# Performance work log

Measured on AMD Instinct MI355X. Metric: run time of the kernel, lower is better.

The kernel has to match this reference:

```python
import jax, jax.numpy as jnp
import numpy as np

B, S, IN, H, NC, WSEG = 2, 256, 80, 128, 40, 64
F2 = 2 * H  # bidirectional LSTM output dim


def setup_inputs() -> dict:
    key = jax.random.key(0)
    it = iter(jax.random.split(key, 48))
    def nrm(shape, scale):
        return jax.random.normal(next(it), shape, jnp.float32) * scale
    d = {}
    d["x"] = jax.random.normal(next(it), (B, S, IN), jnp.float32)
    d["lengths"] = jnp.full((B,), S, dtype=jnp.int32)
    ins = [IN, F2]
    for l in range(2):
        for dr in ("f", "b"):
            sc = 1.0 / np.sqrt(H)
            d[f"w_ih_l{l}{dr}"] = nrm((4 * H, ins[l]), sc)
            d[f"w_hh_l{l}{dr}"] = nrm((4 * H, H), sc)
            d[f"b_l{l}{dr}"] = nrm((4 * H,), sc)
    PD = 3 * F2  # pairwise phi feature dim
    d["a_s0"] = jnp.float32(0.25); d["w_s1"] = nrm((100, PD), 1.0 / np.sqrt(PD)); d["b_s1"] = jnp.zeros((100,), jnp.float32)
    d["a_s1"] = jnp.float32(0.25); d["w_s2"] = nrm((1, 100), 0.1); d["b_s2"] = jnp.zeros((1,), jnp.float32)
    d["a_c0"] = jnp.float32(0.25); d["w_c1"] = nrm((2 * NC, F2), 1.0 / np.sqrt(F2)); d["b_c1"] = jnp.zeros((2 * NC,), jnp.float32)
    d["a_c1"] = jnp.float32(0.25); d["w_c2"] = nrm((NC, 2 * NC), 0.1); d["b_c2"] = jnp.zeros((NC,), jnp.float32)
    d["a_b0"] = jnp.float32(0.25); d["w_b1"] = nrm((2 * NC, F2), 1.0 / np.sqrt(F2)); d["b_b1"] = jnp.zeros((2 * NC,), jnp.float32)
    d["a_b1"] = jnp.float32(0.25); d["w_b2"] = nrm((2, 2 * NC), 0.1); d["b_b2"] = jnp.zeros((2,), jnp.float32)
    return d


def prelu(x, a):
    return jnp.where(x >= 0, x, a * x)


def mlp(x, a0, W1, b1, a1, W2, b2):
    h = prelu(x, a0) @ W1.T + b1
    return prelu(h, a1) @ W2.T + b2


def lstm_dir(x, Wih, Whh, b, reverse):
    # PyTorch gate order: i, f, g, o
    pre = jnp.einsum("bsi,gi->sbg", x, Wih) + b  # [S,B,4H]
    if reverse:
        pre = pre[::-1]
    h0 = jnp.zeros((x.shape[0], Whh.shape[1]), x.dtype)
    def step(carry, xt):
        h, c = carry
        g = xt + h @ Whh.T
        i, f, gg, o = jnp.split(g, 4, axis=-1)
        c = jax.nn.sigmoid(f) * c + jax.nn.sigmoid(i) * jnp.tanh(gg)
        h = jax.nn.sigmoid(o) * jnp.tanh(c)
        return (h, c), h
    _, hs = jax.lax.scan(step, (h0, h0), pre)
    if reverse:
        hs = hs[::-1]
    return jnp.swapaxes(hs, 0, 1)  # [B,S,H]


def encode(x, layers):
    out = x
    for (wif, whf, bf, wib, whb, bb) in layers:
        out = jnp.concatenate([
            lstm_dir(out, wif, whf, bf, False),
            lstm_dir(out, wib, whb, bb, True),
        ], axis=-1)
    return out


def compute_scores(rnn_out, a_s0, w_s1, b_s1, a_s1, w_s2, b_s2):
    cum = jnp.cumsum(rnn_out, axis=1)
    # phi[b,i,j] = [cum[j]-cum[i], out[i], out[j]]  (faithful to calc_phi)
    c = cum[:, None, :, :] - cum[:, :, None, :]
    sh = c.shape
    dmat = jnp.broadcast_to(rnn_out[:, :, None, :], sh)
    emat = jnp.broadcast_to(rnn_out[:, None, :, :], sh)
    phi = jnp.concatenate([c, dmat, emat], axis=-1)  # [B,S,S,3*F2]
    return mlp(phi, a_s0, w_s1, b_s1, a_s1, w_s2, b_s2)[..., 0]  # [B,S,S]


def dp_backptr(scores):
    # Viterbi-style DP: best[i] = max_{j in [i-WSEG, i)} best[j] + scores[:, j, i]
    Bn, Sn = scores.shape[:2]
    def step(best, i):
        start = jnp.maximum(0, i - WSEG)
        jidx = start + jnp.arange(WSEG)
        bwin = jax.lax.dynamic_slice(best, (0, start), (Bn, WSEG))
        swin = jax.lax.dynamic_slice(scores, (0, start, i), (Bn, WSEG, 1))[..., 0]
        cand = jnp.where(jidx[None, :] < i, bwin + swin, -1e9)
        k = (start + jnp.argmax(cand, axis=1)).astype(jnp.int32)
        best = jax.lax.dynamic_update_slice(best, jnp.max(cand, axis=1, keepdims=True), (0, i))
        return best, k
    _, ks = jax.lax.scan(step, jnp.zeros((Bn, Sn), scores.dtype), jnp.arange(1, Sn))
    backptr = jnp.concatenate([jnp.zeros((1, Bn), jnp.int32), ks], axis=0).T  # [B,S]
    return backptr


def backtrack(scores, backptr, lengths):
    Bn, Sn = scores.shape[:2]
    bar = jnp.arange(Bn)
    def step(carry, _):
        cur, acc, bm = carry
        bm = bm.at[bar, cur].set(True)
        prev = backptr[bar, cur]
        active = cur > 0
        acc = acc + jnp.where(active, scores[bar, prev, cur], 0.0)
        cur = jnp.where(active, prev, 0)
        return (cur, acc, bm), None
    init = ((lengths - 1).astype(jnp.int32), jnp.zeros((Bn,), scores.dtype), jnp.zeros((Bn, Sn), bool))
    (_, acc, bm), _ = jax.lax.scan(step, init, None, length=Sn)
    return bm, acc


def reference(x, lengths,
              w_ih_l0f, w_hh_l0f, b_l0f, w_ih_l0b, w_hh_l0b, b_l0b,
              w_ih_l1f, w_hh_l1f, b_l1f, w_ih_l1b, w_hh_l1b, b_l1b,
              a_s0, w_s1, b_s1, a_s1, w_s2, b_s2,
              a_c0, w_c1, b_c1, a_c1, w_c2, b_c2,
              a_b0, w_b1, b_b1, a_b1, w_b2, b_b2):
    layers = [
        (w_ih_l0f, w_hh_l0f, b_l0f, w_ih_l0b, w_hh_l0b, b_l0b),
        (w_ih_l1f, w_hh_l1f, b_l1f, w_ih_l1b, w_hh_l1b, b_l1b),
    ]
    rnn_out = encode(x, layers)  # [B,S,2H]
    cls_out = mlp(rnn_out, a_c0, w_c1, b_c1, a_c1, w_c2, b_c2)
    bin_out = mlp(rnn_out, a_b0, w_b1, b_b1, a_b1, w_b2, b_b2)
    scores = compute_scores(rnn_out, a_s0, w_s1, b_s1, a_s1, w_s2, b_s2)
    backptr = dp_backptr(scores)
    bmask, pred_scores = backtrack(scores, backptr, lengths)
    # bmask[b,i]==1 iff i is a predicted segment boundary (padded-dense encoding of pred lists)
    return cls_out, bin_out, bmask.astype(jnp.int32), pred_scores
```

## Files before the change

### kernel.cpp

```cpp
#include <hip/hip_runtime.h>
#include <math.h>


#define OFF_BIN 20480
#define OFF_BM  21504
#define OFF_PRED 22016

__device__ __forceinline__ float preluf(float x, float a) { return x >= 0.f ? x : a * x; }
__device__ __forceinline__ float sigf(float x) { return 1.f / (1.f + __expf(-x)); }
__device__ __forceinline__ float tanh_fast(float x) { return 1.f - 2.f / (__expf(2.f * x) + 1.f); }

__global__ __launch_bounds__(256) void k_gemm(const float* __restrict__ A,
                                              const float* __restrict__ B,
                                              int Adim, int K,
                                              const float* __restrict__ wf,
                                              const float* __restrict__ bf,
                                              const float* __restrict__ wb,
                                              const float* __restrict__ bbv,
                                              float* __restrict__ outF,
                                              float* __restrict__ outB) {
    int mtile = blockIdx.y;
    int dir = mtile >> 3;
    const float* W = dir ? wb : wf;
    const float* bias = dir ? bbv : bf;
    float* out = dir ? outB : outF;
    int g0 = (mtile & 7) << 6;
    int tb0 = blockIdx.x << 6;
    int tid = threadIdx.x;
    int Bdim = K - Adim;

    __shared__ float Ws[16][68];
    __shared__ float Xs[16][68];

    int r = tid >> 2, c4 = tid & 3;
    int tbr = tb0 + r;
    int hr = ((tbr & 1) << 8) | (tbr >> 1);
    int ty = tid >> 4;
    int tx = tid & 15;
    float acc[4][4] = {};

    for (int k0 = 0; k0 < K; k0 += 16) {
        float4 wv = *(const float4*)(W + (size_t)(g0 + r) * K + k0 + (c4 << 2));
        const float* src = (k0 < Adim) ? (A + (size_t)hr * Adim + k0)
                                       : (B + (size_t)hr * Bdim + (k0 - Adim));
        float4 xv = *(const float4*)(src + (c4 << 2));
        __syncthreads();
        int kc = c4 << 2;
        Ws[kc + 0][r] = wv.x; Ws[kc + 1][r] = wv.y; Ws[kc + 2][r] = wv.z; Ws[kc + 3][r] = wv.w;
        Xs[kc + 0][r] = xv.x; Xs[kc + 1][r] = xv.y; Xs[kc + 2][r] = xv.z; Xs[kc + 3][r] = xv.w;
        __syncthreads();
#pragma unroll
        for (int kk = 0; kk < 16; ++kk) {
            float4 wq = *(const float4*)&Ws[kk][ty << 2];
            float4 xq = *(const float4*)&Xs[kk][tx << 2];
            acc[0][0] += wq.x * xq.x; acc[0][1] += wq.x * xq.y; acc[0][2] += wq.x * xq.z; acc[0][3] += wq.x * xq.w;
            acc[1][0] += wq.y * xq.x; acc[1][1] += wq.y * xq.y; acc[1][2] += wq.y * xq.z; acc[1][3] += wq.y * xq.w;
            acc[2][0] += wq.z * xq.x; acc[2][1] += wq.z * xq.y; acc[2][2] += wq.z * xq.z; acc[2][3] += wq.z * xq.w;
            acc[3][0] += wq.w * xq.x; acc[3][1] += wq.w * xq.y; acc[3][2] += wq.w * xq.z; acc[3][3] += wq.w * xq.w;
        }
    }
    int gq = g0 + (ty << 2);
    float b0 = bias[gq], b1 = bias[gq + 1], b2 = bias[gq + 2], b3 = bias[gq + 3];
#pragma unroll
    for (int j = 0; j < 4; ++j) {
        int tb = tb0 + (tx << 2) + j;
        float4 v = make_float4(acc[0][j] + b0, acc[1][j] + b1, acc[2][j] + b2, acc[3][j] + b3);
        *(float4*)(out + (size_t)tb * 512 + gq) = v;
    }
}

__global__ __launch_bounds__(512, 2) void k_lstm(const float* __restrict__ pre_f,
                                                 const float* __restrict__ pre_b,
                                                 const float* __restrict__ whh_f,
                                                 const float* __restrict__ whh_b,
                                                 float* __restrict__ hout_f,
                                                 float* __restrict__ hout_b) {
    const int dir = blockIdx.x >> 1;
    const int b = blockIdx.x & 1;
    const float* pre = dir ? pre_b : pre_f;
    const float* whh = dir ? whh_b : whh_f;
    float* hout = dir ? hout_b : hout_f;
    const int tid = threadIdx.x;
    const int c = tid >> 7;
    const int gg = tid & 127;
    const int k0 = c << 5;

    float w[4][32];
#pragma unroll
    for (int j = 0; j < 4; ++j) {
#pragma unroll
        for (int k = 0; k < 32; k += 4) {
            float4 v = *(const float4*)(whh + (size_t)((j << 7) + gg) * 128 + k0 + k);
            w[j][k] = v.x; w[j][k + 1] = v.y; w[j][k + 2] = v.z; w[j][k + 3] = v.w;
        }
    }

    __shared__ __align__(16) float hl[128];
    __shared__ float4 part[4][128];
    if (tid < 128) hl[tid] = 0.f;
    float cst = 0.f;
    __syncthreads();

    int t0 = dir ? 255 : 0;
    const float* pp0 = pre + ((size_t)t0 * 2 + b) * 512;
    float p0 = pp0[gg], p1 = pp0[128 + gg], p2 = pp0[256 + gg], p3 = pp0[384 + gg];

    for (int step = 0; step < 256; ++step) {
        int t = dir ? (255 - step) : step;
        float n0 = 0.f, n1 = 0.f, n2 = 0.f, n3 = 0.f;
        if (step < 255) {
            int tn = dir ? (254 - step) : (step + 1);
            const float* pp = pre + ((size_t)tn * 2 + b) * 512;
            n0 = pp[gg]; n1 = pp[128 + gg]; n2 = pp[256 + gg]; n3 = pp[384 + gg];
        }
        float a0 = 0.f, a1 = 0.f, a2 = 0.f, a3 = 0.f;
#pragma unroll
        for (int k = 0; k < 32; k += 4) {
            float4 h4 = *(const float4*)(hl + k0 + k);
            a0 += w[0][k] * h4.x + w[0][k + 1] * h4.y + w[0][k + 2] * h4.z + w[0][k + 3] * h4.w;
            a1 += w[1][k] * h4.x + w[1][k + 1] * h4.y + w[1][k + 2] * h4.z + w[1][k + 3] * h4.w;
            a2 += w[2][k] * h4.x + w[2][k + 1] * h4.y + w[2][k + 2] * h4.z + w[2][k + 3] * h4.w;
            a3 += w[3][k] * h4.x + w[3][k + 1] * h4.y + w[3][k + 2] * h4.z + w[3][k + 3] * h4.w;
        }
        part[c][gg] = make_float4(a0, a1, a2, a3);
        __syncthreads();
        float4 q0 = part[0][gg], q1 = part[1][gg], q2 = part[2][gg], q3 = part[3][gg];
        float gi = p0 + ((q0.x + q1.x) + (q2.x + q3.x));
        float gf = p1 + ((q0.y + q1.y) + (q2.y + q3.y));
        float gG = p2 + ((q0.z + q1.z) + (q2.z + q3.z));
        float go = p3 + ((q0.w + q1.w) + (q2.w + q3.w));
        cst = sigf(gf) * cst + sigf(gi) * tanh_fast(gG);
        float h = sigf(go) * tanh_fast(cst);
        hl[gg] = h;
        if (tid < 128) hout[(size_t)(((b << 8) + t) << 7) + gg] = h;
        p0 = n0; p1 = n1; p2 = n2; p3 = n3;
        __syncthreads();
    }
}

__global__ __launch_bounds__(256) void k_feats(const float* __restrict__ h1f,
                                               const float* __restrict__ h1b,
                                               const float* __restrict__ ws1,
                                               const float* __restrict__ bs1,
                                               const float* a_s0,
                                               float* __restrict__ Pd,
                                               float* __restrict__ Pe,
                                               const float* ac0p, const float* __restrict__ wc1,
                                               const float* __restrict__ bc1, const float* ac1p,
                                               const float* __restrict__ wc2, const float* __restrict__ bc2,
                                               const float* ab0p, const float* __restrict__ wb1,
                                               const float* __restrict__ bb1, const float* ab1p,
                                               const float* __restrict__ wb2, const float* __restrict__ bb2,
                                               float* __restrict__ out,
                                               float* __restrict__ cum) {
    __shared__ __align__(16) float xa[256];
    __shared__ __align__(16) float xb2[256];
    __shared__ __align__(16) float hc[80];
    __shared__ __align__(16) float hb[80];
    int bid = blockIdx.x;
    int tid = threadIdx.x;
    int kk = tid & 127;
    if (bid < 512) {
        int row = bid;
        float a0 = a_s0[0];
        float v = ((tid < 128) ? h1f : h1b)[(size_t)row * 128 + kk];
        xa[tid] = preluf(v, a0);
        __syncthreads();
        const float4* p4 = (const float4*)xa;
        if (tid < 100) {
            const float4* wr = (const float4*)(ws1 + (size_t)tid * 768 + 256);
            float acc = bs1[tid];
#pragma unroll 8
            for (int q = 0; q < 64; ++q) {
                float4 w4 = wr[q], x4 = p4[q];
                acc += w4.x * x4.x + w4.y * x4.y + w4.z * x4.z + w4.w * x4.w;
            }
            Pd[(size_t)row * 100 + tid] = acc;
        } else if (tid >= 128 && tid < 228) {
            int u = tid - 128;
            const float4* wr = (const float4*)(ws1 + (size_t)u * 768 + 512);
            float acc = 0.f;
#pragma unroll 8
            for (int q = 0; q < 64; ++q) {
                float4 w4 = wr[q], x4 = p4[q];
                acc += w4.x * x4.x + w4.y * x4.y + w4.z * x4.z + w4.w * x4.w;
            }
            Pe[(size_t)row * 100 + u] = acc;
        }
    } else if (bid < 1024) {
        int row = bid - 512;
        float ac0 = ac0p[0], ac1 = ac1p[0], ab0 = ab0p[0], ab1 = ab1p[0];
        float v = ((tid < 128) ? h1f : h1b)[(size_t)row * 128 + kk];
        xa[tid] = preluf(v, ac0);
        xb2[tid] = preluf(v, ab0);
        __syncthreads();
        if (tid < 80) {
            const float4* wr = (const float4*)(wc1 + (size_t)tid * 256);
            const float4* x4 = (const float4*)xa;
            float acc = bc1[tid];
#pragma unroll 8
            for (int q = 0; q < 64; ++q) {
                float4 w4 = wr[q], p = x4[q];
                acc += w4.x * p.x + w4.y * p.y + w4.z * p.z + w4.w * p.w;
            }
            hc[tid] = preluf(acc, ac1);
        } else if (tid >= 128 && tid < 208) {
            int u = tid - 128;
            const float4* wr = (const float4*)(wb1 + (size_t)u * 256);
            const float4* x4 = (const float4*)xb2;
            float acc = bb1[u];
#pragma unroll 8
            for (int q = 0; q < 64; ++q) {
                float4 w4 = wr[q], p = x4[q];
                acc += w4.x * p.x + w4.y * p.y + w4.z * p.z + w4.w * p.w;
            }
            hb[u] = preluf(acc, ab1);
        }
        __syncthreads();
        if (tid < 40) {
            const float4* wr = (const float4*)(wc2 + (size_t)tid * 80);
            const float4* h4 = (const float4*)hc;
            float acc = bc2[tid];
#pragma unroll
            for (int q = 0; q < 20; ++q) {
                float4 w4 = wr[q], p = h4[q];
                acc += w4.x * p.x + w4.y * p.y + w4.z * p.z + w4.w * p.w;
            }
            out[(size_t)row * 40 + tid] = acc;
        } else if (tid >= 64 && tid < 66) {
            int j = tid - 64;
            const float4* wr = (const float4*)(wb2 + (size_t)j * 80);
            const float4* h4 = (const float4*)hb;
            float acc = bb2[j];
#pragma unroll
            for (int q = 0; q < 20; ++q) {
                float4 w4 = wr[q], p = h4[q];
                acc += w4.x * p.x + w4.y * p.y + w4.z * p.z + w4.w * p.w;
            }
            out[OFF_BIN + (size_t)row * 2 + j] = acc;
        }
    } else {
        int b = bid - 1024;
        const float* src = (tid < 128) ? h1f : h1b;
        float run = 0.f;
#pragma unroll 8
        for (int t = 0; t < 256; ++t) {
            float v = src[(size_t)(((b << 8) + t) << 7) + kk];
            cum[(size_t)(((b << 8) + t) << 8) + tid] = run + v;
            run += v;
        }
    }
}

__global__ __launch_bounds__(256) void k_scores(const float* __restrict__ cum,
                                                const float* __restrict__ ws1,
                                                const float* __restrict__ ws2,
                                                const float* __restrict__ bs2,
                                                const float* __restrict__ Pd,
                                                const float* __restrict__ Pe,
                                                const float* a_s0p, const float* a_s1p,
                                                float* __restrict__ scT) {
    int bid = blockIdx.x;
    int dt = bid & 3, e = (bid >> 2) & 255, b = bid >> 10;
    int d0 = dt << 6;
    int tid = threadIdx.x;
    __shared__ float cume[256];
    __shared__ float Y[64 * 257];
    __shared__ float red[4][64];
    float a0 = a_s0p[0], a1 = a_s1p[0];
    cume[tid] = cum[(size_t)(((b << 8) + e) << 8) + tid];
    __syncthreads();
#pragma unroll 4
    for (int dj = 0; dj < 64; ++dj) {
        float cd = cum[(size_t)(((b << 8) + (d0 + dj)) << 8) + tid];
        Y[dj * 257 + tid] = preluf(cume[tid] - cd, a0);
    }
    __syncthreads();
    int ug = __builtin_amdgcn_readfirstlane(tid >> 6);
    int ld = tid & 63;
    int d = d0 + ld;
    float acc[25];
#pragma unroll
    for (int t = 0; t < 25; ++t) acc[t] = 0.f;
    const float* wc = ws1 + (size_t)(ug * 25) * 768;
    const float* yrow = Y + ld * 257;
    for (int k = 0; k < 256; k += 4) {
        float y0 = yrow[k], y1 = yrow[k + 1], y2 = yrow[k + 2], y3 = yrow[k + 3];
#pragma unroll
        for (int t = 0; t < 25; ++t) {
            float4 wq = *(const float4*)(wc + (size_t)t * 768 + k);
            acc[t] += y0 * wq.x + y1 * wq.y + y2 * wq.z + y3 * wq.w;
        }
    }
    const float* pdrow = Pd + (size_t)((b << 8) + d) * 100;
    const float* perow = Pe + (size_t)((b << 8) + e) * 100;
    float part = 0.f;
#pragma unroll
    for (int t = 0; t < 25; ++t) {
        int u = ug * 25 + t;
        float h = acc[t] + pdrow[u] + perow[u];
        part += preluf(h, a1) * ws2[u];
    }
    red[ug][ld] = part;
    __syncthreads();
    if (tid < 64) {
        float s = red[0][tid] + red[1][tid] + red[2][tid] + red[3][tid] + bs2[0];
        scT[(size_t)(((b << 8) + e) << 8) + d0 + tid] = s;
    }
}

__global__ __launch_bounds__(128) void k_dp(const float* __restrict__ scT,
                                            const int* __restrict__ lengths,
                                            float* __restrict__ out) {
    __shared__ float best[2][256];
    __shared__ int bp[2][256];
    __shared__ float bm[2][256];
    int tid = threadIdx.x;
    for (int i = tid; i < 512; i += 128) {
        ((float*)best)[i] = 0.f;
        ((int*)bp)[i] = 0;
        ((float*)bm)[i] = 0.f;
    }
    __syncthreads();
    int b = tid >> 6, ln = tid & 63;
    const float* sb = scT + ((size_t)b << 16);
    float sc_next = sb[(1 << 8) + ln];
    for (int i = 1; i < 256; ++i) {
        float sc = sc_next;
        if (i < 255) {
            int i2 = i + 1;
            int st2 = (i2 > 64) ? (i2 - 64) : 0;
            sc_next = sb[(i2 << 8) + st2 + ln];
        }
        int start = (i > 64) ? (i - 64) : 0;
        int j = start + ln;
        float v = -1000000000.0f;
        int ki = j;
        if (j < i) v = best[b][j] + sc;
#pragma unroll
        for (int off = 32; off > 0; off >>= 1) {
            float ov = __shfl_down(v, off);
            int ok = __shfl_down(ki, off);
            if (ov > v || (ov == v && ok < ki)) { v = ov; ki = ok; }
        }
        if (ln == 0) { best[b][i] = v; bp[b][i] = ki; }
    }
    __syncthreads();
    if (tid < 2) {
        int bb = tid;
        int cur = lengths[bb] - 1;
        out[OFF_PRED + bb] = best[bb][cur];
        for (int it = 0; it < 256; ++it) {
            bm[bb][cur] = 1.f;
            int prev = bp[bb][cur];
            cur = (cur > 0) ? prev : 0;
        }
    }
    __syncthreads();
    for (int i = tid; i < 512; i += 128) out[OFF_BM + i] = ((float*)bm)[i];
}

extern "C" void kernel_launch(void* const* d_in, const int* in_sizes, int n_in,
                              void* d_out, int out_size, void* d_ws, size_t ws_size,
                              hipStream_t stream) {
    const float* x     = (const float*)d_in[0];
    const int* lengths = (const int*)d_in[1];
    const float* wih0f = (const float*)d_in[2];
    const float* whh0f = (const float*)d_in[3];
    const float* b0f   = (const float*)d_in[4];
    const float* wih0b = (const float*)d_in[5];
    const float* whh0b = (const float*)d_in[6];
    const float* b0b   = (const float*)d_in[7];
    const float* wih1f = (const float*)d_in[8];
    const float* whh1f = (const float*)d_in[9];
    const float* b1f   = (const float*)d_in[10];
    const float* wih1b = (const float*)d_in[11];
    const float* whh1b = (const float*)d_in[12];
    const float* b1b   = (const float*)d_in[13];
    const float* a_s0  = (const float*)d_in[14];
    const float* w_s1  = (const float*)d_in[15];
    const float* b_s1  = (const float*)d_in[16];
    const float* a_s1  = (const float*)d_in[17];
    const float* w_s2  = (const float*)d_in[18];
    const float* b_s2  = (const float*)d_in[19];
    const float* a_c0  = (const float*)d_in[20];
    const float* w_c1  = (const float*)d_in[21];
    const float* b_c1  = (const float*)d_in[22];
    const float* a_c1  = (const float*)d_in[23];
    const float* w_c2  = (const float*)d_in[24];
    const float* b_c2  = (const float*)d_in[25];
    const float* a_b0  = (const float*)d_in[26];
    const float* w_b1  = (const float*)d_in[27];
    const float* b_b1  = (const float*)d_in[28];
    const float* a_b1  = (const float*)d_in[29];
    const float* w_b2  = (const float*)d_in[30];
    const float* b_b2  = (const float*)d_in[31];

    float* wsf = (float*)d_ws;
    float* preF = wsf;
    float* preB = wsf + 262144;
    float* h0f  = wsf + 524288;
    float* h0b  = wsf + 589824;
    float* h1f  = wsf + 655360;
    float* h1b  = wsf + 720896;
    float* cum  = wsf + 786432;
    float* Pd   = wsf + 917504;
    float* Pe   = wsf + 968704;
    float* scT  = wsf + 1019904;
    float* out  = (float*)d_out;

    k_gemm<<<dim3(8, 16), 256, 0, stream>>>(x, x, 80, 80, wih0f, b0f, wih0b, b0b, preF, preB);
    k_lstm<<<4, 512, 0, stream>>>(preF, preB, whh0f, whh0b, h0f, h0b);
    k_gemm<<<dim3(8, 16), 256, 0, stream>>>(h0f, h0b, 128, 256, wih1f, b1f, wih1b, b1b, preF, preB);
    k_lstm<<<4, 512, 0, stream>>>(preF, preB, whh1f, whh1b, h1f, h1b);
    k_feats<<<1026, 256, 0, stream>>>(h1f, h1b, w_s1, b_s1, a_s0, Pd, Pe,
                                      a_c0, w_c1, b_c1, a_c1, w_c2, b_c2,
                                      a_b0, w_b1, b_b1, a_b1, w_b2, b_b2, out, cum);
    k_scores<<<2048, 256, 0, stream>>>(cum, w_s1, w_s2, b_s2, Pd, Pe, a_s0, a_s1, scT);
    k_dp<<<1, 128, 0, stream>>>(scT, lengths, out);
}
```

Before: 1.025 ms.

## Restructure LSTM recurrence to one gate row per thread with shuffle-based gate combine

Each thread now holds a full 128-wide row of the recurrent weight matrix in registers and computes one gate pre-activation for one hidden unit. The four gates of a unit are combined with cross-lane shuffles, which removes the shared-memory partial-sum reduction. The hidden state is double-buffered in shared memory, so each time step needs one barrier instead of two. This is meant to shorten the latency of the serial 256-step critical path, at the cost of 128 weight registers per thread under a 512-thread, 2-block launch bound, which risks register spills.

```diff
diff --git a/kernel.cpp b/kernel.cpp
--- a/kernel.cpp
+++ b/kernel.cpp
@@ -81,60 +81,59 @@
     const float* whh = dir ? whh_b : whh_f;
     float* hout = dir ? hout_b : hout_f;
     const int tid = threadIdx.x;
-    const int c = tid >> 7;
-    const int gg = tid & 127;
-    const int k0 = c << 5;
-
-    float w[4][32];
-#pragma unroll
-    for (int j = 0; j < 4; ++j) {
-#pragma unroll
-        for (int k = 0; k < 32; k += 4) {
-            float4 v = *(const float4*)(whh + (size_t)((j << 7) + gg) * 128 + k0 + k);
-            w[j][k] = v.x; w[j][k + 1] = v.y; w[j][k + 2] = v.z; w[j][k + 3] = v.w;
-        }
-    }
-
-    __shared__ __align__(16) float hl[128];
-    __shared__ float4 part[4][128];
-    if (tid < 128) hl[tid] = 0.f;
+    const int wv = tid >> 6;
+    const int lane = tid & 63;
+    const int j = lane >> 4;
+    const int uu = (wv << 4) | (lane & 15);
+    const int row = (j << 7) | uu;
+
+    float w[128];
+#pragma unroll
+    for (int k = 0; k < 128; k += 4) {
+        float4 v = *(const float4*)(whh + (size_t)row * 128 + k);
+        w[k] = v.x; w[k + 1] = v.y; w[k + 2] = v.z; w[k + 3] = v.w;
+    }
+
+    __shared__ __align__(16) float hl[2][128];
+    if (tid < 128) hl[0][tid] = 0.f;
     float cst = 0.f;
     __syncthreads();
 
     int t0 = dir ? 255 : 0;
-    const float* pp0 = pre + ((size_t)t0 * 2 + b) * 512;
-    float p0 = pp0[gg], p1 = pp0[128 + gg], p2 = pp0[256 + gg], p3 = pp0[384 + gg];
-
+    float p = pre[((size_t)t0 * 2 + b) * 512 + row];
+
+    int buf = 0;
     for (int step = 0; step < 256; ++step) {
         int t = dir ? (255 - step) : step;
-        float n0 = 0.f, n1 = 0.f, n2 = 0.f, n3 = 0.f;
+        float n = 0.f;
         if (step < 255) {
             int tn = dir ? (254 - step) : (step + 1);
-            const float* pp = pre + ((size_t)tn * 2 + b) * 512;
-            n0 = pp[gg]; n1 = pp[128 + gg]; n2 = pp[256 + gg]; n3 = pp[384 + gg];
-        }
-        float a0 = 0.f, a1 = 0.f, a2 = 0.f, a3 = 0.f;
-#pragma unroll
-        for (int k = 0; k < 32; k += 4) {
-            float4 h4 = *(const float4*)(hl + k0 + k);
-            a0 += w[0][k] * h4.x + w[0][k + 1] * h4.y + w[0][k + 2] * h4.z + w[0][k + 3] * h4.w;
-            a1 += w[1][k] * h4.x + w[1][k + 1] * h4.y + w[1][k + 2] * h4.z + w[1][k + 3] * h4.w;
-            a2 += w[2][k] * h4.x + w[2][k + 1] * h4.y + w[2][k + 2] * h4.z + w[2][k + 3] * h4.w;
-            a3 += w[3][k] * h4.x + w[3][k + 1] * h4.y + w[3][k + 2] * h4.z + w[3][k + 3] * h4.w;
-        }
-        part[c][gg] = make_float4(a0, a1, a2, a3);
-        __syncthreads();
-        float4 q0 = part[0][gg], q1 = part[1][gg], q2 = part[2][gg], q3 = part[3][gg];
-        float gi = p0 + ((q0.x + q1.x) + (q2.x + q3.x));
-        float gf = p1 + ((q0.y + q1.y) + (q2.y + q3.y));
-        float gG = p2 + ((q0.z + q1.z) + (q2.z + q3.z));
-        float go = p3 + ((q0.w + q1.w) + (q2.w + q3.w));
-        cst = sigf(gf) * cst + sigf(gi) * tanh_fast(gG);
-        float h = sigf(go) * tanh_fast(cst);
-        hl[gg] = h;
-        if (tid < 128) hout[(size_t)(((b << 8) + t) << 7) + gg] = h;
-        p0 = n0; p1 = n1; p2 = n2; p3 = n3;
-        __syncthreads();
+            n = pre[((size_t)tn * 2 + b) * 512 + row];
+        }
+        float acc = p;
+#pragma unroll
+        for (int k = 0; k < 128; k += 4) {
+            float4 h4 = *(const float4*)(hl[buf] + k);
+            acc += w[k] * h4.x + w[k + 1] * h4.y + w[k + 2] * h4.z + w[k + 3] * h4.w;
+        }
+        float v = (j == 2) ? tanh_fast(acc) : sigf(acc);
+        float pv = __shfl_xor(v, 32);
+        float a = v * pv;
+        float sf = (j == 1) ? v : pv;
+        float so = (j == 1) ? pv : v;
+        float x1 = __shfl_xor((j & 1) ? sf : a, 16);
+        float x2 = __shfl_xor((j & 1) ? so : a, 16);
+        cst = x1 * cst + a;
+        float h = x2 * tanh_fast(cst);
+        if (j == 0) {
+            hl[buf ^ 1][uu] = h;
+            hout[(size_t)(((b << 8) + t) << 7) + uu] = h;
+        } else if (j == 2) {
+            hl[buf ^ 1][uu] = h;
+        }
+        p = n;
+        __syncthreads();
+        buf ^= 1;
     }
 }
 
```

Result: slower. 1.089 ms (+6.3%).

## Process two end positions per block in scores and use DPP argmax in DP

Applied to the files above, without the earlier changes.

The scores kernel now handles two e rows per block and computes the PReLU pairwise features on the fly from cached cum rows, so each w_s1 float4 load feeds two accumulators and the grid is halved. The DP kernel keeps the sliding window of best values in registers, replaces shuffle-based argmax with DPP row and broadcast ops plus readlane, and drops the shared best array. This trades extra register pressure (50 accumulators) for fewer global weight loads and shorter serial DP steps, and the DPP reduction must keep the same lowest-index tie-break.

```diff
diff --git a/kernel.cpp b/kernel.cpp
--- a/kernel.cpp
+++ b/kernel.cpp
@@ -261,95 +261,141 @@
                                                 const float* a_s0p, const float* a_s1p,
                                                 float* __restrict__ scT) {
     int bid = blockIdx.x;
-    int dt = bid & 3, e = (bid >> 2) & 255, b = bid >> 10;
-    int d0 = dt << 6;
+    int dt = bid & 3, et = (bid >> 2) & 127, b = bid >> 9;
+    int d0 = dt << 6, e0 = et << 1;
     int tid = threadIdx.x;
-    __shared__ float cume[256];
-    __shared__ float Y[64 * 257];
-    __shared__ float red[4][64];
+    __shared__ float cumd[64][260];
+    __shared__ __align__(16) float cume[2][260];
+    __shared__ float red[4][2][64];
     float a0 = a_s0p[0], a1 = a_s1p[0];
-    cume[tid] = cum[(size_t)(((b << 8) + e) << 8) + tid];
-    __syncthreads();
-#pragma unroll 4
-    for (int dj = 0; dj < 64; ++dj) {
-        float cd = cum[(size_t)(((b << 8) + (d0 + dj)) << 8) + tid];
-        Y[dj * 257 + tid] = preluf(cume[tid] - cd, a0);
-    }
-    __syncthreads();
+    {
+        int r = tid >> 2, q = tid & 3;
+        const float4* src = (const float4*)(cum + (size_t)(((b << 8) + (d0 + r)) << 8) + (q << 6));
+        float4* dst = (float4*)&cumd[r][q << 6];
+#pragma unroll
+        for (int x = 0; x < 16; ++x) dst[x] = src[x];
+    }
+    if (tid < 128) {
+        int er = tid >> 6, kq = tid & 63;
+        float4 v = *((const float4*)(cum + (size_t)(((b << 8) + (e0 + er)) << 8)) + kq);
+        *((float4*)&cume[er][0] + kq) = v;
+    }
+    __syncthreads();
+
     int ug = __builtin_amdgcn_readfirstlane(tid >> 6);
     int ld = tid & 63;
-    int d = d0 + ld;
-    float acc[25];
-#pragma unroll
-    for (int t = 0; t < 25; ++t) acc[t] = 0.f;
+    float acc0[25], acc1[25];
+#pragma unroll
+    for (int t = 0; t < 25; ++t) { acc0[t] = 0.f; acc1[t] = 0.f; }
     const float* wc = ws1 + (size_t)(ug * 25) * 768;
-    const float* yrow = Y + ld * 257;
     for (int k = 0; k < 256; k += 4) {
-        float y0 = yrow[k], y1 = yrow[k + 1], y2 = yrow[k + 2], y3 = yrow[k + 3];
+        float4 cd = *(const float4*)&cumd[ld][k];
+        float4 c0 = *(const float4*)&cume[0][k];
+        float4 c1 = *(const float4*)&cume[1][k];
+        float4 y0, y1;
+        y0.x = preluf(c0.x - cd.x, a0); y0.y = preluf(c0.y - cd.y, a0);
+        y0.z = preluf(c0.z - cd.z, a0); y0.w = preluf(c0.w - cd.w, a0);
+        y1.x = preluf(c1.x - cd.x, a0); y1.y = preluf(c1.y - cd.y, a0);
+        y1.z = preluf(c1.z - cd.z, a0); y1.w = preluf(c1.w - cd.w, a0);
 #pragma unroll
         for (int t = 0; t < 25; ++t) {
             float4 wq = *(const float4*)(wc + (size_t)t * 768 + k);
-            acc[t] += y0 * wq.x + y1 * wq.y + y2 * wq.z + y3 * wq.w;
-        }
-    }
-    const float* pdrow = Pd + (size_t)((b << 8) + d) * 100;
-    const float* perow = Pe + (size_t)((b << 8) + e) * 100;
-    float part = 0.f;
-#pragma unroll
-    for (int t = 0; t < 25; ++t) {
-        int u = ug * 25 + t;
-        float h = acc[t] + pdrow[u] + perow[u];
-        part += preluf(h, a1) * ws2[u];
-    }
-    red[ug][ld] = part;
-    __syncthreads();
-    if (tid < 64) {
-        float s = red[0][tid] + red[1][tid] + red[2][tid] + red[3][tid] + bs2[0];
-        scT[(size_t)(((b << 8) + e) << 8) + d0 + tid] = s;
-    }
+            acc0[t] += y0.x * wq.x + y0.y * wq.y + y0.z * wq.z + y0.w * wq.w;
+            acc1[t] += y1.x * wq.x + y1.y * wq.y + y1.z * wq.z + y1.w * wq.w;
+        }
+    }
+    const float* pdrow = Pd + (size_t)((b << 8) + d0 + ld) * 100;
+    {
+        const float* perow = Pe + (size_t)((b << 8) + e0) * 100;
+        float part = 0.f;
+#pragma unroll
+        for (int t = 0; t < 25; ++t) {
+            int u = ug * 25 + t;
+            float h = acc0[t] + pdrow[u] + perow[u];
+            part += preluf(h, a1) * ws2[u];
+        }
+        red[ug][0][ld] = part;
+    }
+    {
+        const float* perow = Pe + (size_t)((b << 8) + e0 + 1) * 100;
+        float part = 0.f;
+#pragma unroll
+        for (int t = 0; t < 25; ++t) {
+            int u = ug * 25 + t;
+            float h = acc1[t] + pdrow[u] + perow[u];
+            part += preluf(h, a1) * ws2[u];
+        }
+        red[ug][1][ld] = part;
+    }
+    __syncthreads();
+    if (tid < 128) {
+        int e = tid >> 6, l2 = tid & 63;
+        float s = red[0][e][l2] + red[1][e][l2] + red[2][e][l2] + red[3][e][l2] + bs2[0];
+        scT[(size_t)(((b << 8) + (e0 + e)) << 8) + d0 + l2] = s;
+    }
+}
+
+__device__ __forceinline__ void argmax_dpp(float& v, int& ki) {
+#define AD_STEP(CTRL, RMASK)                                                                    \
+    {                                                                                           \
+        int mv = __builtin_amdgcn_update_dpp(__float_as_int(v), __float_as_int(v), CTRL, RMASK, 0xf, false); \
+        int mk = __builtin_amdgcn_update_dpp(ki, ki, CTRL, RMASK, 0xf, false);                  \
+        float fv = __int_as_float(mv);                                                          \
+        bool take = (fv > v) || (fv == v && mk < ki);                                           \
+        v = take ? fv : v;                                                                      \
+        ki = take ? mk : ki;                                                                    \
+    }
+    AD_STEP(0x111, 0xf)
+    AD_STEP(0x112, 0xf)
+    AD_STEP(0x114, 0xf)
+    AD_STEP(0x118, 0xf)
+    AD_STEP(0x142, 0xa)
+    AD_STEP(0x143, 0xc)
+#undef AD_STEP
 }
 
 __global__ __launch_bounds__(128) void k_dp(const float* __restrict__ scT,
                                             const int* __restrict__ lengths,
                                             float* __restrict__ out) {
-    __shared__ float best[2][256];
     __shared__ int bp[2][256];
     __shared__ float bm[2][256];
     int tid = threadIdx.x;
     for (int i = tid; i < 512; i += 128) {
-        ((float*)best)[i] = 0.f;
         ((int*)bp)[i] = 0;
         ((float*)bm)[i] = 0.f;
     }
     __syncthreads();
     int b = tid >> 6, ln = tid & 63;
     const float* sb = scT + ((size_t)b << 16);
-    float sc_next = sb[(1 << 8) + ln];
+    int lenm1 = lengths[b] - 1;
+    float wreg = 0.f;
+    float bestFinal = 0.f;
+    int jcur = (ln < 1) ? ln : ln - 64;
+    float sc_next = sb[(1 << 8) + ((jcur < 0) ? 0 : jcur)];
     for (int i = 1; i < 256; ++i) {
         float sc = sc_next;
+        int j = jcur;
         if (i < 255) {
-            int i2 = i + 1;
-            int st2 = (i2 > 64) ? (i2 - 64) : 0;
-            sc_next = sb[(i2 << 8) + st2 + ln];
-        }
-        int start = (i > 64) ? (i - 64) : 0;
-        int j = start + ln;
-        float v = -1000000000.0f;
+            int m2 = (i + 1) & 63;
+            int base2 = (i + 1) - m2;
+            int j2 = (ln < m2) ? (base2 + ln) : (base2 + ln - 64);
+            jcur = j2;
+            sc_next = sb[((i + 1) << 8) + ((j2 < 0) ? 0 : j2)];
+        }
+        float v = (j >= 0) ? (wreg + sc) : -1000000000.0f;
         int ki = j;
-        if (j < i) v = best[b][j] + sc;
-#pragma unroll
-        for (int off = 32; off > 0; off >>= 1) {
-            float ov = __shfl_down(v, off);
-            int ok = __shfl_down(ki, off);
-            if (ov > v || (ov == v && ok < ki)) { v = ov; ki = ok; }
-        }
-        if (ln == 0) { best[b][i] = v; bp[b][i] = ki; }
-    }
+        argmax_dpp(v, ki);
+        float bv = __uint_as_float(__builtin_amdgcn_readlane(__float_as_uint(v), 63));
+        int bk = __builtin_amdgcn_readlane(ki, 63);
+        if (ln == (i & 63)) wreg = bv;
+        if (ln == 0) bp[b][i] = bk;
+        if (i == lenm1) bestFinal = bv;
+    }
+    if (ln == 0) out[OFF_PRED + b] = bestFinal;
     __syncthreads();
     if (tid < 2) {
         int bb = tid;
         int cur = lengths[bb] - 1;
-        out[OFF_PRED + bb] = best[bb][cur];
         for (int it = 0; it < 256; ++it) {
             bm[bb][cur] = 1.f;
             int prev = bp[bb][cur];
@@ -416,6 +462,6 @@
     k_feats<<<1026, 256, 0, stream>>>(h1f, h1b, w_s1, b_s1, a_s0, Pd, Pe,
                                       a_c0, w_c1, b_c1, a_c1, w_c2, b_c2,
                                       a_b0, w_b1, b_b1, a_b1, w_b2, b_b2, out, cum);
-    k_scores<<<2048, 256, 0, stream>>>(cum, w_s1, w_s2, b_s2, Pd, Pe, a_s0, a_s1, scT);
+    k_scores<<<1024, 256, 0, stream>>>(cum, w_s1, w_s2, b_s2, Pd, Pe, a_s0, a_s1, scT);
     k_dp<<<1, 128, 0, stream>>>(scT, lengths, out);
 }
```

Result: slower. 1.068 ms (+4.2%).
